# Performance work log

Hardware: AMD Instinct MI355X
Metric: run time of the kernel (lower is better)

The kernel has to match this reference:

```python
import jax, jax.numpy as jnp
import numpy as np

TOP_K = 2

def setup_inputs() -> dict:
    key = jax.random.key(0)
    ks = jax.random.split(key, 5)
    B, S, H, F, E = 4, 512, 1024, 3584, 8
    x = jax.random.normal(ks[0], (B, S, H), dtype=jnp.float32)
    gate_w = jax.random.normal(ks[1], (H, E), dtype=jnp.float32) * (1.0 / np.sqrt(H))
    w1 = jax.random.normal(ks[2], (E, F, H), dtype=jnp.float32) * (1.0 / np.sqrt(H))
    w3 = jax.random.normal(ks[3], (E, F, H), dtype=jnp.float32) * (1.0 / np.sqrt(H))
    w2 = jax.random.normal(ks[4], (E, H, F), dtype=jnp.float32) * (1.0 / np.sqrt(F))
    return {"x": x, "gate_w": gate_w, "w1": w1, "w3": w3, "w2": w2}


def reference(x, gate_w, w1, w3, w2):
    # MoE top-2 routing (Mixtral-style), dense-dispatch formulation.
    B, S, H = x.shape
    E = gate_w.shape[1]
    xt = x.reshape(-1, H)                      # [T, H] flattened tokens
    T = xt.shape[0]
    logits = xt @ gate_w                       # [T, E] gate logits
    top_w, top_i = jax.lax.top_k(logits, TOP_K)    # [T, K]
    top_w = jax.nn.softmax(top_w, axis=-1)         # softmax over selected-k logits
    # combine[t, e] = routing weight of expert e for token t (0 if not selected)
    combine = jnp.zeros((T, E), dtype=xt.dtype)
    combine = combine.at[jnp.arange(T)[:, None], top_i].add(top_w)
    # SwiGLU experts: y_e = w2_e @ (silu(w1_e x) * (w3_e x))
    h = jnp.einsum('th,efh->tef', xt, w1)      # [T, E, F]
    g = jnp.einsum('th,efh->tef', xt, w3)      # [T, E, F]
    act = jax.nn.silu(h) * g                   # [T, E, F]
    out_e = jnp.einsum('tef,ehf->teh', act, w2)  # [T, E, H]
    out = jnp.einsum('teh,te->th', out_e, combine)  # weighted combine over experts
    return out.reshape(B, S, H)
```

## Files before the change

kernel.cpp:

```cpp
#include <hip/hip_runtime.h>
#include <hip/hip_bf16.h>
#include <stdint.h>

#define TOKENS 2048
#define HDIM 1024
#define FDIM 3584
#define NEXP 8
#define BK 32

typedef __attribute__((ext_vector_type(8))) short short8;
typedef __attribute__((ext_vector_type(4))) float floatx4;

#define AS1 __attribute__((address_space(1)))
#define AS3 __attribute__((address_space(3)))

__device__ __forceinline__ void glds16(const void* g, void* l) {
  __builtin_amdgcn_global_load_lds((const AS1 void*)g, (AS3 void*)l, 16, 0, 0);
}

__device__ __forceinline__ unsigned short f2bf(float f) {
  union { float f; unsigned int u; } c; c.f = f;
  unsigned int u = c.u;
  u += 0x7fffu + ((u >> 16) & 1u);
  return (unsigned short)(u >> 16);
}

__device__ __forceinline__ unsigned int pk2bf(float a, float b) {
  __hip_bfloat162 h = __float22bfloat162_rn(make_float2(a, b));
  union { __hip_bfloat162 h; unsigned int u; } c; c.h = h;
  return c.u;
}

__global__ void gate_kernel(const float* __restrict__ x,
                            const float* __restrict__ gw,
                            int* __restrict__ top_e,
                            float* __restrict__ top_w) {
  int wv = threadIdx.x >> 6;
  int lane = threadIdx.x & 63;
  int t = blockIdx.x * 4 + wv;
  if (t >= TOKENS) return;
  float p[NEXP];
#pragma unroll
  for (int e = 0; e < NEXP; e++) p[e] = 0.f;
  const float* xr = x + (size_t)t * HDIM;
  for (int h = lane; h < HDIM; h += 64) {
    float xv = xr[h];
    const float4* g4 = (const float4*)(gw + (size_t)h * NEXP);
    float4 a = g4[0], b = g4[1];
    p[0] += xv * a.x; p[1] += xv * a.y; p[2] += xv * a.z; p[3] += xv * a.w;
    p[4] += xv * b.x; p[5] += xv * b.y; p[6] += xv * b.z; p[7] += xv * b.w;
  }
#pragma unroll
  for (int e = 0; e < NEXP; e++) {
#pragma unroll
    for (int off = 32; off > 0; off >>= 1) p[e] += __shfl_xor(p[e], off, 64);
  }
  if (lane == 0) {
    int i0 = 0;
    for (int e = 1; e < NEXP; e++) if (p[e] > p[i0]) i0 = e;
    int i1 = (i0 == 0) ? 1 : 0;
    for (int e = 0; e < NEXP; e++) if (e != i0 && p[e] > p[i1]) i1 = e;
    float l0 = p[i0], l1 = p[i1];
    float e1 = __expf(l1 - l0);
    float s = 1.f + e1;
    top_e[t * 2] = i0; top_e[t * 2 + 1] = i1;
    top_w[t * 2] = 1.f / s; top_w[t * 2 + 1] = e1 / s;
  }
}

__global__ void route_kernel(const int* __restrict__ top_e,
                             int* __restrict__ count,
                             int* __restrict__ offs,
                             int* __restrict__ tok_of,
                             int* __restrict__ slot_of) {
  __shared__ int hist[NEXP];
  __shared__ int cur[NEXP];
  int tid = threadIdx.x;
  if (tid < NEXP) hist[tid] = 0;
  __syncthreads();
  int e[4];
#pragma unroll
  for (int j = 0; j < 4; j++) {
    int i = tid * 4 + j;
    e[j] = top_e[i];
    atomicAdd(&hist[e[j]], 1);
  }
  __syncthreads();
  if (tid == 0) {
    int o = 0;
    for (int k = 0; k < NEXP; k++) {
      offs[k] = o; cur[k] = o; count[k] = hist[k]; o += hist[k];
    }
  }
  __syncthreads();
#pragma unroll
  for (int j = 0; j < 4; j++) {
    int i = tid * 4 + j;
    int g = atomicAdd(&cur[e[j]], 1);
    tok_of[g] = i >> 1;
    slot_of[i] = g;
  }
}

__global__ void xconv_kernel(const float* __restrict__ x,
                             unsigned short* __restrict__ xbf) {
  int i = (blockIdx.x * blockDim.x + threadIdx.x) * 4;
  float4 v = *(const float4*)(x + i);
  uint2 pk;
  pk.x = pk2bf(v.x, v.y);
  pk.y = pk2bf(v.z, v.w);
  *(uint2*)(xbf + i) = pk;
}

__global__ void wconv_kernel(const float* __restrict__ w1,
                             const float* __restrict__ w3,
                             const float* __restrict__ w2,
                             unsigned short* __restrict__ b1,
                             unsigned short* __restrict__ b3,
                             unsigned short* __restrict__ b2) {
  int z = blockIdx.y;
  const float* src = (z == 0) ? w1 : (z == 1) ? w3 : w2;
  unsigned short* dst = (z == 0) ? b1 : (z == 1) ? b3 : b2;
  size_t i = ((size_t)blockIdx.x * 256 + threadIdx.x) * 8;
  float4 a = *(const float4*)(src + i);
  float4 b = *(const float4*)(src + i + 4);
  uint4 o;
  o.x = pk2bf(a.x, a.y); o.y = pk2bf(a.z, a.w);
  o.z = pk2bf(b.x, b.y); o.w = pk2bf(b.z, b.w);
  *(uint4*)(dst + i) = o;
}

#define G1_BM 128
#define G1_BF 64

__global__ __launch_bounds__(256, 3)
void gemm1_kernel(const unsigned short* __restrict__ xbf,
                  const unsigned short* __restrict__ w1b,
                  const unsigned short* __restrict__ w3b,
                  const int* __restrict__ count,
                  const int* __restrict__ offs,
                  const int* __restrict__ tok_of,
                  unsigned short* __restrict__ act) {
  int e = blockIdx.z;
  int cnt = count[e];
  int m0 = blockIdx.y * G1_BM;
  if (m0 >= cnt) return;
  int f0 = blockIdx.x * G1_BF;
  int off_e = offs[e];

  __shared__ __align__(16) unsigned short sA[G1_BM * 32];
  __shared__ __align__(16) unsigned short sB1[G1_BF * 32];
  __shared__ __align__(16) unsigned short sB3[G1_BF * 32];

  int tid = threadIdx.x;
  int lane = tid & 63, wv = tid >> 6;

  const unsigned short* ag[2];
  char* alb[2];
#pragma unroll
  for (int p = 0; p < 2; p++) {
    int c = tid + p * 256;
    int row = c >> 2, slot = c & 3;
    int gch = slot ^ ((row >> 1) & 3);
    int r = m0 + row;
    int tok = tok_of[off_e + (r < cnt ? r : 0)];
    ag[p] = xbf + (size_t)tok * HDIM + gch * 8;
    alb[p] = (char*)sA + (wv * 64 + p * 256) * 16;
  }
  const unsigned short *b1g, *b3g;
  char *b1l, *b3l;
  {
    int row = tid >> 2, slot = tid & 3;
    int gch = slot ^ ((row >> 1) & 3);
    size_t wrow = (size_t)e * FDIM + f0 + row;
    b1g = w1b + wrow * HDIM + gch * 8;
    b3g = w3b + wrow * HDIM + gch * 8;
    b1l = (char*)sB1 + (wv * 64) * 16;
    b3l = (char*)sB3 + (wv * 64) * 16;
  }

  int lrow = lane & 15, quad = lane >> 4;
  int wm = wv >> 1, wn = wv & 1;

  floatx4 acc1[4][2], acc3[4][2];
#pragma unroll
  for (int i = 0; i < 4; i++)
#pragma unroll
    for (int j = 0; j < 2; j++) {
      acc1[i][j] = (floatx4){0.f, 0.f, 0.f, 0.f};
      acc3[i][j] = (floatx4){0.f, 0.f, 0.f, 0.f};
    }

  for (int k0 = 0; k0 < HDIM; k0 += BK) {
    __syncthreads();
#pragma unroll
    for (int p = 0; p < 2; p++) glds16(ag[p] + k0, alb[p]);
    glds16(b1g + k0, b1l);
    glds16(b3g + k0, b3l);
    __syncthreads();

    short8 af[4], b1f[2], b3f[2];
#pragma unroll
    for (int ms = 0; ms < 4; ms++) {
      int r = wm * 64 + ms * 16 + lrow;
      int sl = quad ^ ((r >> 1) & 3);
      af[ms] = *(const short8*)(sA + r * 32 + sl * 8);
    }
#pragma unroll
    for (int ns = 0; ns < 2; ns++) {
      int r = wn * 32 + ns * 16 + lrow;
      int sl = quad ^ ((r >> 1) & 3);
      b1f[ns] = *(const short8*)(sB1 + r * 32 + sl * 8);
      b3f[ns] = *(const short8*)(sB3 + r * 32 + sl * 8);
    }
#pragma unroll
    for (int ms = 0; ms < 4; ms++)
#pragma unroll
      for (int ns = 0; ns < 2; ns++) {
        acc1[ms][ns] = __builtin_amdgcn_mfma_f32_16x16x32_bf16(af[ms], b1f[ns], acc1[ms][ns], 0, 0, 0);
        acc3[ms][ns] = __builtin_amdgcn_mfma_f32_16x16x32_bf16(af[ms], b3f[ns], acc3[ms][ns], 0, 0, 0);
      }
  }

#pragma unroll
  for (int ms = 0; ms < 4; ms++) {
#pragma unroll
    for (int reg = 0; reg < 4; reg++) {
      int slot = m0 + wm * 64 + ms * 16 + quad * 4 + reg;
      if (slot < cnt) {
        unsigned short* ar = act + (size_t)(off_e + slot) * FDIM + f0 + wn * 32;
#pragma unroll
        for (int ns = 0; ns < 2; ns++) {
          float h = acc1[ms][ns][reg];
          float g = acc3[ms][ns][reg];
          float a = h / (1.f + __expf(-h)) * g;
          ar[ns * 16 + lrow] = f2bf(a);
        }
      }
    }
  }
}

#define G2_BM 128
#define G2_BN 128
#define SPLITK 4
#define G2_KS (FDIM / SPLITK)

__global__ __launch_bounds__(256, 3)
void gemm2_kernel(const unsigned short* __restrict__ act,
                  const unsigned short* __restrict__ w2b,
                  const int* __restrict__ count,
                  const int* __restrict__ offs,
                  float* __restrict__ part) {
  int zz = blockIdx.z;
  int e = zz & 7, sk = zz >> 3;
  int cnt = count[e];
  int m0 = blockIdx.y * G2_BM;
  if (m0 >= cnt) return;
  int h0 = blockIdx.x * G2_BN;
  int off_e = offs[e];
  int kb = sk * G2_KS;

  __shared__ __align__(16) unsigned short sA[G2_BM * 32];
  __shared__ __align__(16) unsigned short sB[G2_BN * 32];

  int tid = threadIdx.x;
  int lane = tid & 63, wv = tid >> 6;

  const unsigned short* ag[2];
  char* alb[2];
#pragma unroll
  for (int p = 0; p < 2; p++) {
    int c = tid + p * 256;
    int row = c >> 2, slot = c & 3;
    int gch = slot ^ ((row >> 1) & 3);
    int r = m0 + row;
    int rr = (r < cnt ? r : 0);
    ag[p] = act + (size_t)(off_e + rr) * FDIM + kb + gch * 8;
    alb[p] = (char*)sA + (wv * 64 + p * 256) * 16;
  }
  const unsigned short* bg[2];
  char* blb[2];
#pragma unroll
  for (int p = 0; p < 2; p++) {
    int c = tid + p * 256;
    int row = c >> 2, slot = c & 3;
    int gch = slot ^ ((row >> 1) & 3);
    bg[p] = w2b + ((size_t)e * HDIM + h0 + row) * FDIM + kb + gch * 8;
    blb[p] = (char*)sB + (wv * 64 + p * 256) * 16;
  }

  int lrow = lane & 15, quad = lane >> 4;
  int wm = wv >> 1, wn = wv & 1;

  floatx4 acc[4][4];
#pragma unroll
  for (int i = 0; i < 4; i++)
#pragma unroll
    for (int j = 0; j < 4; j++) acc[i][j] = (floatx4){0.f, 0.f, 0.f, 0.f};

  for (int k0 = 0; k0 < G2_KS; k0 += BK) {
    __syncthreads();
#pragma unroll
    for (int p = 0; p < 2; p++) glds16(ag[p] + k0, alb[p]);
#pragma unroll
    for (int p = 0; p < 2; p++) glds16(bg[p] + k0, blb[p]);
    __syncthreads();

    short8 af[4], bf[4];
#pragma unroll
    for (int ms = 0; ms < 4; ms++) {
      int r = wm * 64 + ms * 16 + lrow;
      int sl = quad ^ ((r >> 1) & 3);
      af[ms] = *(const short8*)(sA + r * 32 + sl * 8);
    }
#pragma unroll
    for (int ns = 0; ns < 4; ns++) {
      int r = wn * 64 + ns * 16 + lrow;
      int sl = quad ^ ((r >> 1) & 3);
      bf[ns] = *(const short8*)(sB + r * 32 + sl * 8);
    }
#pragma unroll
    for (int ms = 0; ms < 4; ms++)
#pragma unroll
      for (int ns = 0; ns < 4; ns++)
        acc[ms][ns] = __builtin_amdgcn_mfma_f32_16x16x32_bf16(af[ms], bf[ns], acc[ms][ns], 0, 0, 0);
  }

#pragma unroll
  for (int ms = 0; ms < 4; ms++) {
#pragma unroll
    for (int reg = 0; reg < 4; reg++) {
      int slot = m0 + wm * 64 + ms * 16 + quad * 4 + reg;
      if (slot < cnt) {
        float* crow = part + ((size_t)sk * 4096 + off_e + slot) * HDIM + h0 + wn * 64;
#pragma unroll
        for (int ns = 0; ns < 4; ns++)
          crow[ns * 16 + lrow] = acc[ms][ns][reg];
      }
    }
  }
}

__global__ void combine_kernel(const float* __restrict__ part,
                               const int* __restrict__ slot_of,
                               const float* __restrict__ top_w,
                               float* __restrict__ out) {
  int t = blockIdx.x;
  int g0 = slot_of[t * 2], g1 = slot_of[t * 2 + 1];
  float w0 = top_w[t * 2], w1 = top_w[t * 2 + 1];
  int i = threadIdx.x;
  float4 s0 = {0.f, 0.f, 0.f, 0.f}, s1 = {0.f, 0.f, 0.f, 0.f};
#pragma unroll
  for (int sk = 0; sk < SPLITK; sk++) {
    float4 a = ((const float4*)(part + ((size_t)sk * 4096 + g0) * HDIM))[i];
    float4 b = ((const float4*)(part + ((size_t)sk * 4096 + g1) * HDIM))[i];
    s0.x += a.x; s0.y += a.y; s0.z += a.z; s0.w += a.w;
    s1.x += b.x; s1.y += b.y; s1.z += b.z; s1.w += b.w;
  }
  float4 r;
  r.x = w0 * s0.x + w1 * s1.x;
  r.y = w0 * s0.y + w1 * s1.y;
  r.z = w0 * s0.z + w1 * s1.z;
  r.w = w0 * s0.w + w1 * s1.w;
  ((float4*)(out + (size_t)t * HDIM))[i] = r;
}

extern "C" void kernel_launch(void* const* d_in, const int* in_sizes, int n_in,
                              void* d_out, int out_size, void* d_ws, size_t ws_size,
                              hipStream_t stream) {
  const float* x  = (const float*)d_in[0];
  const float* gw = (const float*)d_in[1];
  const float* w1 = (const float*)d_in[2];
  const float* w3 = (const float*)d_in[3];
  const float* w2 = (const float*)d_in[4];
  float* out = (float*)d_out;

  char* ws = (char*)d_ws;
  const size_t MB = 1ull << 20;
  float* top_w = (float*)(ws);
  int* top_e   = (int*)(ws + 16384);
  int* slot_of = (int*)(ws + 32768);
  int* tok_of  = (int*)(ws + 49152);
  int* count   = (int*)(ws + 65536);
  int* offs    = (int*)(ws + 65536 + 64);

  unsigned short* xbf = (unsigned short*)(ws + 1 * MB);
  unsigned short* act = (unsigned short*)(ws + 5 * MB);
  unsigned short* w2b = (unsigned short*)(ws + 35 * MB);
  unsigned short* w1b = (unsigned short*)(ws + 94 * MB);
  unsigned short* w3b = (unsigned short*)(ws + 150 * MB);
  float* part = (float*)(ws + 94 * MB);

  gate_kernel<<<TOKENS / 4, 256, 0, stream>>>(x, gw, top_e, top_w);
  route_kernel<<<1, 1024, 0, stream>>>(top_e, count, offs, tok_of, slot_of);
  xconv_kernel<<<(TOKENS * HDIM) / (256 * 4), 256, 0, stream>>>(x, xbf);
  wconv_kernel<<<dim3(14336, 3), 256, 0, stream>>>(w1, w3, w2, w1b, w3b, w2b);
  gemm1_kernel<<<dim3(FDIM / G1_BF, TOKENS / G1_BM, NEXP), 256, 0, stream>>>(
      xbf, w1b, w3b, count, offs, tok_of, act);
  gemm2_kernel<<<dim3(HDIM / G2_BN, TOKENS / G2_BM, NEXP * SPLITK), 256, 0, stream>>>(
      act, w2b, count, offs, part);
  combine_kernel<<<TOKENS, 256, 0, stream>>>(part, slot_of, top_w, out);
}
```

Baseline: 528.9 us.

## Double-buffer LDS tiles in both expert GEMMs, halve split-K, grid-stride weight conversion

Both expert GEMMs now double-buffer their shared-memory tiles, issuing the next K-slice's global-to-LDS loads before the MFMAs on the current slice. This cuts one barrier per iteration and overlaps load latency with compute. The down-projection split-K drops from 4 to 2, which halves the partial-sum traffic but launches fewer blocks. The weight conversion kernel becomes a grid-stride loop with fewer blocks, and the doubled LDS per block may reduce occupancy.

```diff
diff --git a/kernel.cpp b/kernel.cpp
--- a/kernel.cpp
+++ b/kernel.cpp
@@ -112,6 +112,8 @@
   *(uint2*)(xbf + i) = pk;
 }
 
+#define WCONV_N (29360128ull)
+#define WCONV_BLK 3584
 __global__ void wconv_kernel(const float* __restrict__ w1,
                              const float* __restrict__ w3,
                              const float* __restrict__ w2,
@@ -121,13 +123,17 @@
   int z = blockIdx.y;
   const float* src = (z == 0) ? w1 : (z == 1) ? w3 : w2;
   unsigned short* dst = (z == 0) ? b1 : (z == 1) ? b3 : b2;
-  size_t i = ((size_t)blockIdx.x * 256 + threadIdx.x) * 8;
-  float4 a = *(const float4*)(src + i);
-  float4 b = *(const float4*)(src + i + 4);
-  uint4 o;
-  o.x = pk2bf(a.x, a.y); o.y = pk2bf(a.z, a.w);
-  o.z = pk2bf(b.x, b.y); o.w = pk2bf(b.z, b.w);
-  *(uint4*)(dst + i) = o;
+  int t4 = threadIdx.x * 4;
+  for (size_t base = (size_t)blockIdx.x * 2048; base < WCONV_N;
+       base += (size_t)WCONV_BLK * 2048) {
+    float4 a = *(const float4*)(src + base + t4);
+    float4 b = *(const float4*)(src + base + 1024 + t4);
+    uint2 pa, pb;
+    pa.x = pk2bf(a.x, a.y); pa.y = pk2bf(a.z, a.w);
+    pb.x = pk2bf(b.x, b.y); pb.y = pk2bf(b.z, b.w);
+    *(uint2*)(dst + base + t4) = pa;
+    *(uint2*)(dst + base + 1024 + t4) = pb;
+  }
 }
 
 #define G1_BM 128
@@ -148,9 +154,9 @@
   int f0 = blockIdx.x * G1_BF;
   int off_e = offs[e];
 
-  __shared__ __align__(16) unsigned short sA[G1_BM * 32];
-  __shared__ __align__(16) unsigned short sB1[G1_BF * 32];
-  __shared__ __align__(16) unsigned short sB3[G1_BF * 32];
+  __shared__ __align__(16) unsigned short sA[2 * G1_BM * 32];
+  __shared__ __align__(16) unsigned short sB1[2 * G1_BF * 32];
+  __shared__ __align__(16) unsigned short sB3[2 * G1_BF * 32];
 
   int tid = threadIdx.x;
   int lane = tid & 63, wv = tid >> 6;
@@ -191,27 +197,42 @@
       acc3[i][j] = (floatx4){0.f, 0.f, 0.f, 0.f};
     }
 
-  for (int k0 = 0; k0 < HDIM; k0 += BK) {
-    __syncthreads();
-#pragma unroll
-    for (int p = 0; p < 2; p++) glds16(ag[p] + k0, alb[p]);
-    glds16(b1g + k0, b1l);
-    glds16(b3g + k0, b3l);
-    __syncthreads();
+  const int NT = HDIM / BK;
+
+#pragma unroll
+  for (int p = 0; p < 2; p++) glds16(ag[p], alb[p]);
+  glds16(b1g, b1l);
+  glds16(b3g, b3l);
+  __syncthreads();
+
+  int cur = 0;
+  for (int t = 0; t < NT; t++) {
+    if (t + 1 < NT) {
+      int k = (t + 1) * BK;
+      int nb = cur ^ 1;
+#pragma unroll
+      for (int p = 0; p < 2; p++) glds16(ag[p] + k, alb[p] + nb * 8192);
+      glds16(b1g + k, b1l + nb * 4096);
+      glds16(b3g + k, b3l + nb * 4096);
+    }
+
+    const unsigned short* sAc = sA + cur * (G1_BM * 32);
+    const unsigned short* sB1c = sB1 + cur * (G1_BF * 32);
+    const unsigned short* sB3c = sB3 + cur * (G1_BF * 32);
 
     short8 af[4], b1f[2], b3f[2];
 #pragma unroll
     for (int ms = 0; ms < 4; ms++) {
       int r = wm * 64 + ms * 16 + lrow;
       int sl = quad ^ ((r >> 1) & 3);
-      af[ms] = *(const short8*)(sA + r * 32 + sl * 8);
+      af[ms] = *(const short8*)(sAc + r * 32 + sl * 8);
     }
 #pragma unroll
     for (int ns = 0; ns < 2; ns++) {
       int r = wn * 32 + ns * 16 + lrow;
       int sl = quad ^ ((r >> 1) & 3);
-      b1f[ns] = *(const short8*)(sB1 + r * 32 + sl * 8);
-      b3f[ns] = *(const short8*)(sB3 + r * 32 + sl * 8);
+      b1f[ns] = *(const short8*)(sB1c + r * 32 + sl * 8);
+      b3f[ns] = *(const short8*)(sB3c + r * 32 + sl * 8);
     }
 #pragma unroll
     for (int ms = 0; ms < 4; ms++)
@@ -220,6 +241,9 @@
         acc1[ms][ns] = __builtin_amdgcn_mfma_f32_16x16x32_bf16(af[ms], b1f[ns], acc1[ms][ns], 0, 0, 0);
         acc3[ms][ns] = __builtin_amdgcn_mfma_f32_16x16x32_bf16(af[ms], b3f[ns], acc3[ms][ns], 0, 0, 0);
       }
+
+    __syncthreads();
+    cur ^= 1;
   }
 
 #pragma unroll
@@ -243,7 +267,7 @@
 
 #define G2_BM 128
 #define G2_BN 128
-#define SPLITK 4
+#define SPLITK 2
 #define G2_KS (FDIM / SPLITK)
 
 __global__ __launch_bounds__(256, 3)
@@ -261,8 +285,8 @@
   int off_e = offs[e];
   int kb = sk * G2_KS;
 
-  __shared__ __align__(16) unsigned short sA[G2_BM * 32];
-  __shared__ __align__(16) unsigned short sB[G2_BN * 32];
+  __shared__ __align__(16) unsigned short sA[2 * G2_BM * 32];
+  __shared__ __align__(16) unsigned short sB[2 * G2_BN * 32];
 
   int tid = threadIdx.x;
   int lane = tid & 63, wv = tid >> 6;
@@ -299,32 +323,48 @@
 #pragma unroll
     for (int j = 0; j < 4; j++) acc[i][j] = (floatx4){0.f, 0.f, 0.f, 0.f};
 
-  for (int k0 = 0; k0 < G2_KS; k0 += BK) {
-    __syncthreads();
-#pragma unroll
-    for (int p = 0; p < 2; p++) glds16(ag[p] + k0, alb[p]);
-#pragma unroll
-    for (int p = 0; p < 2; p++) glds16(bg[p] + k0, blb[p]);
-    __syncthreads();
+  const int NT = G2_KS / BK;
+
+#pragma unroll
+  for (int p = 0; p < 2; p++) { glds16(ag[p], alb[p]); glds16(bg[p], blb[p]); }
+  __syncthreads();
+
+  int cur = 0;
+  for (int t = 0; t < NT; t++) {
+    if (t + 1 < NT) {
+      int k = (t + 1) * BK;
+      int nb = cur ^ 1;
+#pragma unroll
+      for (int p = 0; p < 2; p++) {
+        glds16(ag[p] + k, alb[p] + nb * 8192);
+        glds16(bg[p] + k, blb[p] + nb * 8192);
+      }
+    }
+
+    const unsigned short* sAc = sA + cur * (G2_BM * 32);
+    const unsigned short* sBc = sB + cur * (G2_BN * 32);
 
     short8 af[4], bf[4];
 #pragma unroll
     for (int ms = 0; ms < 4; ms++) {
       int r = wm * 64 + ms * 16 + lrow;
       int sl = quad ^ ((r >> 1) & 3);
-      af[ms] = *(const short8*)(sA + r * 32 + sl * 8);
+      af[ms] = *(const short8*)(sAc + r * 32 + sl * 8);
     }
 #pragma unroll
     for (int ns = 0; ns < 4; ns++) {
       int r = wn * 64 + ns * 16 + lrow;
       int sl = quad ^ ((r >> 1) & 3);
-      bf[ns] = *(const short8*)(sB + r * 32 + sl * 8);
+      bf[ns] = *(const short8*)(sBc + r * 32 + sl * 8);
     }
 #pragma unroll
     for (int ms = 0; ms < 4; ms++)
 #pragma unroll
       for (int ns = 0; ns < 4; ns++)
         acc[ms][ns] = __builtin_amdgcn_mfma_f32_16x16x32_bf16(af[ms], bf[ns], acc[ms][ns], 0, 0, 0);
+
+    __syncthreads();
+    cur ^= 1;
   }
 
 #pragma unroll
@@ -395,7 +435,7 @@
   gate_kernel<<<TOKENS / 4, 256, 0, stream>>>(x, gw, top_e, top_w);
   route_kernel<<<1, 1024, 0, stream>>>(top_e, count, offs, tok_of, slot_of);
   xconv_kernel<<<(TOKENS * HDIM) / (256 * 4), 256, 0, stream>>>(x, xbf);
-  wconv_kernel<<<dim3(14336, 3), 256, 0, stream>>>(w1, w3, w2, w1b, w3b, w2b);
+  wconv_kernel<<<dim3(WCONV_BLK, 3), 256, 0, stream>>>(w1, w3, w2, w1b, w3b, w2b);
   gemm1_kernel<<<dim3(FDIM / G1_BF, TOKENS / G1_BM, NEXP), 256, 0, stream>>>(
       xbf, w1b, w3b, count, offs, tok_of, act);
   gemm2_kernel<<<dim3(HDIM / G2_BN, TOKENS / G2_BM, NEXP * SPLITK), 256, 0, stream>>>(
```

Result: no change. 534.7 us (+1.1%).
